# Optimization experiments

Hardware: AMD Instinct MI355X
Metric: run time of the kernel (lower is better)

The kernel has to match this reference:

```python
import jax, jax.numpy as jnp
import numpy as np

N = 50000      # nodes
E = 800000     # random edges (self-loops added in reference, per PyG GATConv default)
F_IN = 128
B = 512        # graphs in the batch
NEG_SLOPE = 0.2  # PyG GATConv leaky_relu default


def setup_inputs() -> dict:
    key = jax.random.key(0)
    ks = jax.random.split(key, 12)
    def w(k, shape, fan_in):
        return jax.random.normal(k, shape, jnp.float32) / np.sqrt(fan_in)
    return {
        "x": jax.random.normal(ks[0], (N, F_IN), jnp.float32),
        "edge_index": jax.random.randint(ks[1], (2, E), 0, N, dtype=jnp.int32),
        "batch": jnp.sort(jax.random.randint(ks[2], (N,), 0, B, dtype=jnp.int32)),
        "W1": w(ks[3], (F_IN, 4 * 64), F_IN),
        "a_src1": w(ks[4], (4, 64), 64),
        "a_dst1": w(ks[5], (4, 64), 64),
        "b1": jnp.zeros((4 * 64,), jnp.float32),
        "W2": w(ks[6], (256, 1 * 128), 256),
        "a_src2": w(ks[7], (1, 128), 128),
        "a_dst2": w(ks[8], (1, 128), 128),
        "b2": jnp.zeros((128,), jnp.float32),
        "Wl": w(ks[9], (128, 1), 128),
        "bl": jnp.zeros((1,), jnp.float32),
    }


def gat_layer(x, src, dst, W, a_src, a_dst, b, n):
    H, Fo = a_src.shape
    h = (x @ W).reshape(n, H, Fo)                      # [N,H,Fo]
    alpha_s = jnp.einsum("nhf,hf->nh", h, a_src)       # [N,H]
    alpha_d = jnp.einsum("nhf,hf->nh", h, a_dst)
    e = jax.nn.leaky_relu(alpha_s[src] + alpha_d[dst], NEG_SLOPE)  # [E,H]
    # segment softmax over incoming edges of each dst node
    m = jax.ops.segment_max(e, dst, num_segments=n)    # [N,H]; self-loops => every node hit
    ex = jnp.exp(e - m[dst])
    den = jax.ops.segment_sum(ex, dst, num_segments=n)
    alpha = ex / den[dst]                              # [E,H]
    out = jax.ops.segment_sum(h[src] * alpha[:, :, None], dst, num_segments=n)
    return out.reshape(n, H * Fo) + b


def reference(x, edge_index, batch, W1, a_src1, a_dst1, b1, W2, a_src2, a_dst2, b2, Wl, bl):
    n = x.shape[0]
    loops = jnp.arange(n, dtype=edge_index.dtype)
    src = jnp.concatenate([edge_index[0], loops])
    dst = jnp.concatenate([edge_index[1], loops])
    h = jax.nn.elu(gat_layer(x, src, dst, W1, a_src1, a_dst1, b1, n))
    h = jax.nn.elu(gat_layer(h, src, dst, W2, a_src2, a_dst2, b2, n))
    # dropout omitted (inference)
    sums = jax.ops.segment_sum(h, batch, num_segments=B)
    cnt = jax.ops.segment_sum(jnp.ones((n,), h.dtype), batch, num_segments=B)
    g = sums / jnp.maximum(cnt, 1.0)[:, None]          # global_mean_pool -> [B,128]
    return jax.nn.sigmoid(g @ Wl + bl).reshape(-1)     # [B]
```

## Files before the change

kernel.cpp:

```cpp
#include <hip/hip_runtime.h>
#include <hip/hip_bf16.h>

#define NN 50000
#define EE 800000
#define ETOT 850000
#define BB 512
#define CAP 64

typedef __hip_bfloat16 bf16;
typedef __attribute__((ext_vector_type(8))) __bf16 v8bf;
typedef __attribute__((ext_vector_type(4))) float f32x4;

__device__ __forceinline__ float lo2f(unsigned int u) {
    return __uint_as_float(u << 16);
}
__device__ __forceinline__ float hi2f(unsigned int u) {
    return __uint_as_float(u & 0xffff0000u);
}
__device__ __forceinline__ unsigned short f2bfbits(float f) {
    bf16 h = __float2bfloat16(f);
    return *reinterpret_cast<unsigned short*>(&h);
}
__device__ __forceinline__ float lrelu_exp(float ev) {
    ev = ev > 0.f ? ev : 0.2f * ev;
    return __expf(fminf(ev, 80.f));
}

__global__ void k_init(int* __restrict__ deg, float* __restrict__ pooled,
                       int* __restrict__ cnt) {
    int i = blockIdx.x * blockDim.x + threadIdx.x;
    if (i < NN) deg[i] = 0;
    if (i < BB * 128) pooled[i] = 0.f;
    if (i < BB) cnt[i] = 0;
}

__global__ void k_scatter(const int* __restrict__ srcArr, const int* __restrict__ dstArr,
                          int* __restrict__ deg, int* __restrict__ csrc) {
    int e = blockIdx.x * blockDim.x + threadIdx.x;
    if (e >= ETOT) return;
    int d, s;
    if (e < EE) { d = dstArr[e]; s = srcArr[e]; }
    else        { d = e - EE;    s = d; }
    d = min(max(d, 0), NN - 1);
    s = min(max(s, 0), NN - 1);
    int p = atomicAdd(&deg[d], 1);
    if (p < CAP) csrc[d * CAP + p] = s;
}

__global__ void k_cvtw(const float* __restrict__ W1, const float* __restrict__ W2,
                       bf16* __restrict__ wt1, bf16* __restrict__ wt2,
                       const int* __restrict__ batch, int* __restrict__ cnt) {
    int idx = blockIdx.x * blockDim.x + threadIdx.x;
    if (idx < 256 * 128) {
        int c = idx >> 7, k = idx & 127;
        wt1[idx] = __float2bfloat16(W1[k * 256 + c]);
    } else {
        int j = idx - 256 * 128;
        int c = j >> 8, k = j & 255;
        wt2[j] = __float2bfloat16(W2[k * 128 + c]);
    }
    if (idx < NN) {
        int g = batch[idx];
        g = min(max(g, 0), BB - 1);
        atomicAdd(&cnt[g], 1);
    }
}

__global__ __launch_bounds__(256, 2)
void k_gemm1(const float* __restrict__ x, const bf16* __restrict__ wt1,
             const float* __restrict__ aw_s, const float* __restrict__ aw_d,
             bf16* __restrict__ h1, float* __restrict__ as1,
             float* __restrict__ ad1) {
    int n0 = blockIdx.x * 32;
    int t = threadIdx.x;
    __shared__ bf16 xs[32 * 136];
    for (int i = 0; i < 4; i++) {
        int idx = t + 256 * i;
        int r = idx >> 5, c4 = idx & 31;
        float4 v = make_float4(0.f, 0.f, 0.f, 0.f);
        if (n0 + r < NN) v = *(const float4*)(x + (size_t)(n0 + r) * 128 + c4 * 4);
        ushort4 o;
        o.x = f2bfbits(v.x); o.y = f2bfbits(v.y);
        o.z = f2bfbits(v.z); o.w = f2bfbits(v.w);
        *(ushort4*)(&xs[r * 136 + c4 * 4]) = o;
    }
    __syncthreads();

    int wv = t >> 6, lane = t & 63;
    int q = lane >> 4, r16 = lane & 15;
    int rowBase = (wv & 1) * 16;
    int colBase = (wv >> 1) * 128;

    f32x4 acc[8];
#pragma unroll
    for (int ct = 0; ct < 8; ct++) acc[ct] = (f32x4){0.f, 0.f, 0.f, 0.f};

#pragma unroll
    for (int kt = 0; kt < 4; kt++) {
        v8bf va = *(const v8bf*)(&xs[(rowBase + r16) * 136 + kt * 32 + q * 8]);
#pragma unroll
        for (int ct = 0; ct < 8; ct++) {
            v8bf vb = *(const v8bf*)(wt1 + (size_t)(colBase + ct * 16 + r16) * 128 + kt * 32 + q * 8);
            acc[ct] = __builtin_amdgcn_mfma_f32_16x16x32_bf16(va, vb, acc[ct], 0, 0, 0);
        }
    }

    float wsv[8], wdv[8];
#pragma unroll
    for (int ct = 0; ct < 8; ct++) {
        int col = colBase + ct * 16 + r16;
        wsv[ct] = aw_s[col];
        wdv[ct] = aw_d[col];
    }

    float ps[4][2], pd[4][2];
#pragma unroll
    for (int reg = 0; reg < 4; reg++) {
        ps[reg][0] = 0.f; ps[reg][1] = 0.f;
        pd[reg][0] = 0.f; pd[reg][1] = 0.f;
    }

#pragma unroll
    for (int reg = 0; reg < 4; reg++) {
        int node = n0 + rowBase + q * 4 + reg;
        bool ok = node < NN;
#pragma unroll
        for (int ct = 0; ct < 8; ct++) {
            float v = acc[ct][reg];
            if (ok) h1[(size_t)node * 256 + colBase + ct * 16 + r16] = __float2bfloat16(v);
            ps[reg][ct >> 2] += v * wsv[ct];
            pd[reg][ct >> 2] += v * wdv[ct];
        }
    }

#pragma unroll
    for (int reg = 0; reg < 4; reg++) {
        int node = n0 + rowBase + q * 4 + reg;
        bool ok = node < NN;
#pragma unroll
        for (int lh = 0; lh < 2; lh++) {
            float a = ps[reg][lh], b = pd[reg][lh];
            for (int mask = 1; mask <= 8; mask <<= 1) {
                a += __shfl_xor(a, mask);
                b += __shfl_xor(b, mask);
            }
            if (r16 == 0 && ok) {
                int head = (wv >> 1) * 2 + lh;
                as1[node * 4 + head] = a;
                ad1[node * 4 + head] = b;
            }
        }
    }
}

__global__ void k_gather1(const int* __restrict__ csrc, const int* __restrict__ deg,
                          const bf16* __restrict__ h1, const float* __restrict__ as1,
                          const float* __restrict__ ad1, const float* __restrict__ b1,
                          bf16* __restrict__ x2) {
    int bid = blockIdx.x;
    int n = bid >> 1, slice = bid & 1;
    int t = threadIdx.x;
    int lh = t >> 5;
    int cnt = min(deg[n], CAP);
    float2 ad = *(const float2*)&ad1[n * 4 + slice * 2];
    __shared__ unsigned int ls[CAP];
    __shared__ float la[CAP * 2];
    const char* h1c = (const char*)h1;
    unsigned int tconst = (unsigned int)(slice * 128 + t * 2) * 2;
    if (t < cnt) {
        int s = csrc[n * CAP + t];
        s = min(max(s, 0), NN - 1);
        ls[t] = (unsigned int)s << 9;
        float2 as = *(const float2*)&as1[s * 4 + slice * 2];
        la[t * 2 + 0] = lrelu_exp(as.x + ad.x);
        la[t * 2 + 1] = lrelu_exp(as.y + ad.y);
    }
    __syncthreads();
    float a0 = 0.f, a1 = 0.f, ssum = 0.f;
    int j = 0;
    for (; j + 3 < cnt; j += 4) {
        unsigned int o0 = ls[j] + tconst, o1 = ls[j + 1] + tconst;
        unsigned int o2 = ls[j + 2] + tconst, o3 = ls[j + 3] + tconst;
        float A0 = la[j * 2 + lh], A1 = la[j * 2 + 2 + lh];
        float A2 = la[j * 2 + 4 + lh], A3 = la[j * 2 + 6 + lh];
        unsigned int u0 = *(const unsigned int*)(h1c + o0);
        unsigned int u1 = *(const unsigned int*)(h1c + o1);
        unsigned int u2 = *(const unsigned int*)(h1c + o2);
        unsigned int u3 = *(const unsigned int*)(h1c + o3);
        ssum += (A0 + A1) + (A2 + A3);
        a0 = fmaf(A0, lo2f(u0), a0); a0 = fmaf(A1, lo2f(u1), a0);
        a0 = fmaf(A2, lo2f(u2), a0); a0 = fmaf(A3, lo2f(u3), a0);
        a1 = fmaf(A0, hi2f(u0), a1); a1 = fmaf(A1, hi2f(u1), a1);
        a1 = fmaf(A2, hi2f(u2), a1); a1 = fmaf(A3, hi2f(u3), a1);
    }
    for (; j < cnt; j++) {
        unsigned int o0 = ls[j] + tconst;
        float A0 = la[j * 2 + lh];
        unsigned int u0 = *(const unsigned int*)(h1c + o0);
        ssum += A0;
        a0 = fmaf(A0, lo2f(u0), a0);
        a1 = fmaf(A0, hi2f(u0), a1);
    }
    float inv = 1.f / fmaxf(ssum, 1e-35f);
    int c = slice * 128 + t * 2;
    float r0 = a0 * inv + b1[c + 0];
    float r1 = a1 * inv + b1[c + 1];
    r0 = r0 > 0.f ? r0 : (__expf(r0) - 1.f);
    r1 = r1 > 0.f ? r1 : (__expf(r1) - 1.f);
    unsigned int packed = (unsigned int)f2bfbits(r0) | ((unsigned int)f2bfbits(r1) << 16);
    *(unsigned int*)((unsigned short*)x2 + (size_t)n * 256 + c) = packed;
}

__global__ __launch_bounds__(256, 2)
void k_gemm2(const bf16* __restrict__ x2, const bf16* __restrict__ wt2,
             const float* __restrict__ aw_s, const float* __restrict__ aw_d,
             bf16* __restrict__ h2, float* __restrict__ as2,
             float* __restrict__ ad2) {
    int n0 = blockIdx.x * 32;
    int t = threadIdx.x;
    __shared__ bf16 xs[32 * 264];
    __shared__ float psPart[32][2];
    __shared__ float pdPart[32][2];
    for (int i = 0; i < 4; i++) {
        int idx = t + 256 * i;
        int r = idx >> 5, c8 = idx & 31;
        uint4 v;
        if (n0 + r < NN) v = *(const uint4*)(x2 + (size_t)(n0 + r) * 256 + c8 * 8);
        else             v = make_uint4(0, 0, 0, 0);
        *(uint4*)(&xs[r * 264 + c8 * 8]) = v;
    }
    __syncthreads();

    int wv = t >> 6, lane = t & 63;
    int q = lane >> 4, r16 = lane & 15;
    int rowBase = (wv & 1) * 16;
    int colBase = (wv >> 1) * 64;

    f32x4 acc[4];
#pragma unroll
    for (int ct = 0; ct < 4; ct++) acc[ct] = (f32x4){0.f, 0.f, 0.f, 0.f};

#pragma unroll
    for (int kt = 0; kt < 8; kt++) {
        v8bf va = *(const v8bf*)(&xs[(rowBase + r16) * 264 + kt * 32 + q * 8]);
#pragma unroll
        for (int ct = 0; ct < 4; ct++) {
            v8bf vb = *(const v8bf*)(wt2 + (size_t)(colBase + ct * 16 + r16) * 256 + kt * 32 + q * 8);
            acc[ct] = __builtin_amdgcn_mfma_f32_16x16x32_bf16(va, vb, acc[ct], 0, 0, 0);
        }
    }

    float wsv[4], wdv[4];
#pragma unroll
    for (int ct = 0; ct < 4; ct++) {
        int col = colBase + ct * 16 + r16;
        wsv[ct] = aw_s[col];
        wdv[ct] = aw_d[col];
    }

#pragma unroll
    for (int reg = 0; reg < 4; reg++) {
        int node = n0 + rowBase + q * 4 + reg;
        bool ok = node < NN;
        float ps = 0.f, pd = 0.f;
#pragma unroll
        for (int ct = 0; ct < 4; ct++) {
            float v = acc[ct][reg];
            if (ok) h2[(size_t)node * 128 + colBase + ct * 16 + r16] = __float2bfloat16(v);
            ps += v * wsv[ct];
            pd += v * wdv[ct];
        }
        for (int mask = 1; mask <= 8; mask <<= 1) {
            ps += __shfl_xor(ps, mask);
            pd += __shfl_xor(pd, mask);
        }
        if (r16 == 0) {
            int li = rowBase + q * 4 + reg;
            psPart[li][wv >> 1] = ps;
            pdPart[li][wv >> 1] = pd;
        }
    }
    __syncthreads();
    if (t < 32) {
        int node = n0 + t;
        if (node < NN) {
            as2[node] = psPart[t][0] + psPart[t][1];
            ad2[node] = pdPart[t][0] + pdPart[t][1];
        }
    }
}

__global__ void k_gather2(const int* __restrict__ csrc, const int* __restrict__ deg,
                          const bf16* __restrict__ h2, const float* __restrict__ as2,
                          const float* __restrict__ ad2, const float* __restrict__ b2,
                          const int* __restrict__ batch, float* __restrict__ pooled) {
    int n = blockIdx.x;
    int t = threadIdx.x;
    int cnt = min(deg[n], CAP);
    float adn = ad2[n];
    __shared__ unsigned int ls[CAP];
    __shared__ float la[CAP];
    const char* h2c = (const char*)h2;
    unsigned int tconst = (unsigned int)t * 4;
    if (t < cnt) {
        int s = csrc[n * CAP + t];
        s = min(max(s, 0), NN - 1);
        ls[t] = (unsigned int)s << 8;
        la[t] = lrelu_exp(as2[s] + adn);
    }
    __syncthreads();
    float a0 = 0.f, a1 = 0.f, ssum = 0.f;
    int j = 0;
    for (; j + 3 < cnt; j += 4) {
        unsigned int o0 = ls[j] + tconst, o1 = ls[j + 1] + tconst;
        unsigned int o2 = ls[j + 2] + tconst, o3 = ls[j + 3] + tconst;
        float A0 = la[j], A1 = la[j + 1], A2 = la[j + 2], A3 = la[j + 3];
        unsigned int u0 = *(const unsigned int*)(h2c + o0);
        unsigned int u1 = *(const unsigned int*)(h2c + o1);
        unsigned int u2 = *(const unsigned int*)(h2c + o2);
        unsigned int u3 = *(const unsigned int*)(h2c + o3);
        ssum += (A0 + A1) + (A2 + A3);
        a0 = fmaf(A0, lo2f(u0), a0); a0 = fmaf(A1, lo2f(u1), a0);
        a0 = fmaf(A2, lo2f(u2), a0); a0 = fmaf(A3, lo2f(u3), a0);
        a1 = fmaf(A0, hi2f(u0), a1); a1 = fmaf(A1, hi2f(u1), a1);
        a1 = fmaf(A2, hi2f(u2), a1); a1 = fmaf(A3, hi2f(u3), a1);
    }
    for (; j < cnt; j++) {
        unsigned int o0 = ls[j] + tconst;
        float A0 = la[j];
        unsigned int u0 = *(const unsigned int*)(h2c + o0);
        ssum += A0;
        a0 = fmaf(A0, lo2f(u0), a0);
        a1 = fmaf(A0, hi2f(u0), a1);
    }
    float inv = 1.f / fmaxf(ssum, 1e-35f);
    int c = t * 2;
    float r0 = a0 * inv + b2[c + 0];
    float r1 = a1 * inv + b2[c + 1];
    r0 = r0 > 0.f ? r0 : (__expf(r0) - 1.f);
    r1 = r1 > 0.f ? r1 : (__expf(r1) - 1.f);
    int b = batch[n];
    b = min(max(b, 0), BB - 1);
    atomicAdd(&pooled[b * 128 + c + 0], r0);
    atomicAdd(&pooled[b * 128 + c + 1], r1);
}

__global__ void k_final(const float* __restrict__ pooled, const int* __restrict__ cnt,
                        const float* __restrict__ Wl, const float* __restrict__ bl,
                        float* __restrict__ out) {
    int b = blockIdx.x * blockDim.x + threadIdx.x;
    if (b >= BB) return;
    float acc = 0.f;
    for (int k = 0; k < 128; k++) acc += pooled[b * 128 + k] * Wl[k];
    int c = cnt[b];
    float cf = (float)(c > 0 ? c : 1);
    float g = acc / cf + bl[0];
    out[b] = 1.f / (1.f + __expf(-g));
}

extern "C" void kernel_launch(void* const* d_in, const int* in_sizes, int n_in,
                              void* d_out, int out_size, void* d_ws, size_t ws_size,
                              hipStream_t stream) {
    const float* x = (const float*)d_in[0];
    const int* ei = (const int*)d_in[1];
    const int* batch = (const int*)d_in[2];
    const float* W1 = (const float*)d_in[3];
    const float* aw_s1 = (const float*)d_in[4];
    const float* aw_d1 = (const float*)d_in[5];
    const float* b1 = (const float*)d_in[6];
    const float* W2 = (const float*)d_in[7];
    const float* aw_s2 = (const float*)d_in[8];
    const float* aw_d2 = (const float*)d_in[9];
    const float* b2 = (const float*)d_in[10];
    const float* Wl = (const float*)d_in[11];
    const float* bl = (const float*)d_in[12];
    const int* srcArr = ei;
    const int* dstArr = ei + EE;

    char* w = (char*)d_ws;
    size_t off = 0;
    auto alloc = [&](size_t bytes) -> void* {
        void* p = (void*)(w + off);
        off = (off + bytes + 255) & ~(size_t)255;
        return p;
    };
    bf16* bufA = (bf16*)alloc((size_t)NN * 256 * 2);
    bf16* bufB = (bf16*)alloc((size_t)NN * 256 * 2);
    int* csrc = (int*)alloc((size_t)NN * CAP * 4);
    float* as1 = (float*)alloc((size_t)NN * 4 * 4);
    float* ad1 = (float*)alloc((size_t)NN * 4 * 4);
    float* as2 = (float*)alloc((size_t)NN * 4);
    float* ad2 = (float*)alloc((size_t)NN * 4);
    int* deg = (int*)alloc((size_t)NN * 4);
    bf16* wt1 = (bf16*)alloc((size_t)256 * 128 * 2);
    bf16* wt2 = (bf16*)alloc((size_t)128 * 256 * 2);
    float* pooled = (float*)alloc((size_t)BB * 128 * 4);
    int* cnt = (int*)alloc((size_t)BB * 4);
    (void)ws_size;

    k_init<<<256, 256, 0, stream>>>(deg, pooled, cnt);
    k_scatter<<<(ETOT + 255) / 256, 256, 0, stream>>>(srcArr, dstArr, deg, csrc);
    k_cvtw<<<256, 256, 0, stream>>>(W1, W2, wt1, wt2, batch, cnt);

    bf16* h1 = bufA;
    bf16* x2 = bufB;
    k_gemm1<<<(NN + 31) / 32, 256, 0, stream>>>(x, wt1, aw_s1, aw_d1, h1, as1, ad1);
    k_gather1<<<NN * 2, 64, 0, stream>>>(csrc, deg, h1, as1, ad1, b1, x2);

    bf16* h2 = bufA;
    k_gemm2<<<(NN + 31) / 32, 256, 0, stream>>>(x2, wt2, aw_s2, aw_d2, h2, as2, ad2);

    k_gather2<<<NN, 64, 0, stream>>>(csrc, deg, h2, as2, ad2, b2, batch, pooled);

    k_final<<<2, 256, 0, stream>>>(pooled, cnt, Wl, bl, (float*)d_out);
}
```

Baseline: 372.4 us.

## Replace atomic global mean pooling with a segmented per-graph pooling kernel

The second gather kernel no longer scatters its ELU outputs into per-graph sums with float atomics. It writes them to a dense fp32 node-feature buffer instead. A new kernel then gives each graph its own block, binary-searches the sorted batch array for that graph's node range, and sums, averages and projects the rows before the sigmoid. This also drops the per-graph count atomics and the old final kernel. The aim is to remove heavy atomic contention on 64K pooled addresses. In exchange it adds a full fp32 write and re-read of node features, a serial per-block loop over each graph's rows, and a dependence on batch being sorted.

```diff
diff --git a/kernel.cpp b/kernel.cpp
--- a/kernel.cpp
+++ b/kernel.cpp
@@ -26,12 +26,9 @@
     return __expf(fminf(ev, 80.f));
 }
 
-__global__ void k_init(int* __restrict__ deg, float* __restrict__ pooled,
-                       int* __restrict__ cnt) {
+__global__ void k_init(int* __restrict__ deg) {
     int i = blockIdx.x * blockDim.x + threadIdx.x;
     if (i < NN) deg[i] = 0;
-    if (i < BB * 128) pooled[i] = 0.f;
-    if (i < BB) cnt[i] = 0;
 }
 
 __global__ void k_scatter(const int* __restrict__ srcArr, const int* __restrict__ dstArr,
@@ -48,8 +45,7 @@
 }
 
 __global__ void k_cvtw(const float* __restrict__ W1, const float* __restrict__ W2,
-                       bf16* __restrict__ wt1, bf16* __restrict__ wt2,
-                       const int* __restrict__ batch, int* __restrict__ cnt) {
+                       bf16* __restrict__ wt1, bf16* __restrict__ wt2) {
     int idx = blockIdx.x * blockDim.x + threadIdx.x;
     if (idx < 256 * 128) {
         int c = idx >> 7, k = idx & 127;
@@ -58,11 +54,6 @@
         int j = idx - 256 * 128;
         int c = j >> 8, k = j & 255;
         wt2[j] = __float2bfloat16(W2[k * 128 + c]);
-    }
-    if (idx < NN) {
-        int g = batch[idx];
-        g = min(max(g, 0), BB - 1);
-        atomicAdd(&cnt[g], 1);
     }
 }
 
@@ -293,7 +284,7 @@
 __global__ void k_gather2(const int* __restrict__ csrc, const int* __restrict__ deg,
                           const bf16* __restrict__ h2, const float* __restrict__ as2,
                           const float* __restrict__ ad2, const float* __restrict__ b2,
-                          const int* __restrict__ batch, float* __restrict__ pooled) {
+                          float* __restrict__ hf) {
     int n = blockIdx.x;
     int t = threadIdx.x;
     int cnt = min(deg[n], CAP);
@@ -339,23 +330,33 @@
     float r1 = a1 * inv + b2[c + 1];
     r0 = r0 > 0.f ? r0 : (__expf(r0) - 1.f);
     r1 = r1 > 0.f ? r1 : (__expf(r1) - 1.f);
-    int b = batch[n];
-    b = min(max(b, 0), BB - 1);
-    atomicAdd(&pooled[b * 128 + c + 0], r0);
-    atomicAdd(&pooled[b * 128 + c + 1], r1);
-}
-
-__global__ void k_final(const float* __restrict__ pooled, const int* __restrict__ cnt,
-                        const float* __restrict__ Wl, const float* __restrict__ bl,
-                        float* __restrict__ out) {
-    int b = blockIdx.x * blockDim.x + threadIdx.x;
-    if (b >= BB) return;
-    float acc = 0.f;
-    for (int k = 0; k < 128; k++) acc += pooled[b * 128 + k] * Wl[k];
-    int c = cnt[b];
-    float cf = (float)(c > 0 ? c : 1);
-    float g = acc / cf + bl[0];
-    out[b] = 1.f / (1.f + __expf(-g));
+    *(float2*)(hf + (size_t)n * 128 + c) = make_float2(r0, r1);
+}
+
+__global__ void k_pool(const float* __restrict__ hf, const int* __restrict__ batch,
+                       const float* __restrict__ Wl, const float* __restrict__ bl,
+                       float* __restrict__ out) {
+    int b = blockIdx.x;
+    int t = threadIdx.x;
+    int lo = 0, hi = NN;
+    while (lo < hi) { int m = (lo + hi) >> 1; if (batch[m] < b) lo = m + 1; else hi = m; }
+    int start = lo;
+    int lo2 = start, hi2 = NN;
+    while (lo2 < hi2) { int m = (lo2 + hi2) >> 1; if (batch[m] < b + 1) lo2 = m + 1; else hi2 = m; }
+    int end = lo2;
+    float sum = 0.f;
+    for (int n = start; n < end; n++) sum += hf[(size_t)n * 128 + t];
+    int c = end - start;
+    float g = sum / (float)(c > 0 ? c : 1);
+    float p = g * Wl[t];
+    for (int o = 32; o > 0; o >>= 1) p += __shfl_down(p, o);
+    __shared__ float red[2];
+    if ((t & 63) == 0) red[t >> 6] = p;
+    __syncthreads();
+    if (t == 0) {
+        float acc = red[0] + red[1] + bl[0];
+        out[b] = 1.f / (1.f + __expf(-acc));
+    }
 }
 
 extern "C" void kernel_launch(void* const* d_in, const int* in_sizes, int n_in,
@@ -394,13 +395,11 @@
     int* deg = (int*)alloc((size_t)NN * 4);
     bf16* wt1 = (bf16*)alloc((size_t)256 * 128 * 2);
     bf16* wt2 = (bf16*)alloc((size_t)128 * 256 * 2);
-    float* pooled = (float*)alloc((size_t)BB * 128 * 4);
-    int* cnt = (int*)alloc((size_t)BB * 4);
     (void)ws_size;
 
-    k_init<<<256, 256, 0, stream>>>(deg, pooled, cnt);
+    k_init<<<(NN + 255) / 256, 256, 0, stream>>>(deg);
     k_scatter<<<(ETOT + 255) / 256, 256, 0, stream>>>(srcArr, dstArr, deg, csrc);
-    k_cvtw<<<256, 256, 0, stream>>>(W1, W2, wt1, wt2, batch, cnt);
+    k_cvtw<<<256, 256, 0, stream>>>(W1, W2, wt1, wt2);
 
     bf16* h1 = bufA;
     bf16* x2 = bufB;
@@ -410,7 +409,8 @@
     bf16* h2 = bufA;
     k_gemm2<<<(NN + 31) / 32, 256, 0, stream>>>(x2, wt2, aw_s2, aw_d2, h2, as2, ad2);
 
-    k_gather2<<<NN, 64, 0, stream>>>(csrc, deg, h2, as2, ad2, b2, batch, pooled);
-
-    k_final<<<2, 256, 0, stream>>>(pooled, cnt, Wl, bl, (float*)d_out);
-}
+    float* hf = (float*)bufB;
+    k_gather2<<<NN, 64, 0, stream>>>(csrc, deg, h2, as2, ad2, b2, hf);
+
+    k_pool<<<BB, 128, 0, stream>>>(hf, batch, Wl, bl, (float*)d_out);
+}
```

After: 344.0 us. -7.6%, faster.
